# Kernel optimization log

Hardware: AMD Instinct MI355X
Metric: run time of the kernel (lower is better)

The kernel has to match this reference:

```python
import jax, jax.numpy as jnp
import numpy as np

B, N_IN, N_OUT = 16, 7000, 28000
C_IN, C_OUT, S = 64, 64, 9
NNZ = 3 * N_OUT  # ~3 source verts per upsampled vert (barycentric)


def setup_inputs() -> dict:
    key = jax.random.key(0)
    k = jax.random.split(key, 6)
    x = jax.random.normal(k[0], (B, N_IN, C_IN), dtype=jnp.float32)
    values = jax.random.uniform(k[1], (NNZ,), dtype=jnp.float32)
    row = jax.random.randint(k[2], (NNZ,), 0, N_OUT)
    col = jax.random.randint(k[3], (NNZ,), 0, N_IN)
    spiral_indices = jax.random.randint(k[4], (N_OUT, S), 0, N_OUT)
    weight = jax.random.normal(k[5], (S * C_IN, C_OUT), dtype=jnp.float32) * 0.02
    bias = jnp.zeros((C_OUT,), dtype=jnp.float32)
    return {"x": x, "values": values, "weight": weight, "bias": bias,
            "row": row, "col": col, "spiral_indices": spiral_indices}


def reference(x, values, weight, bias, row, col, spiral_indices):
    # Pool: gather source verts, scale by sparse matrix values, scatter-add to output verts
    n_out = spiral_indices.shape[0]
    gathered = x[:, col, :] * values[None, :, None]            # [B, nnz, C]
    pooled = jnp.zeros((x.shape[0], n_out, x.shape[2]), x.dtype).at[:, row, :].add(gathered)  # [B, N_out, C]
    # SpiralConv: gather spiral neighborhood, flatten, linear
    feat = pooled[:, spiral_indices.reshape(-1), :]            # [B, N_out*S, C]
    feat = feat.reshape(x.shape[0], n_out, -1)                 # [B, N_out, S*C]
    out = jax.nn.elu(jnp.einsum('bnf,fo->bno', feat, weight) + bias)
    return out
```

## Files before the change

kernel.cpp:

```cpp
#include <hip/hip_runtime.h>
#include <math.h>

#define B      16
#define N_IN   7000
#define N_OUT  28000
#define C      64
#define S      9
#define NNZ    (3 * N_OUT)
#define F      (S * C)
#define KB     (F / 32)

#define MT     110

typedef short bf16x8 __attribute__((ext_vector_type(8)));
typedef float f32x4  __attribute__((ext_vector_type(4)));

static __device__ __forceinline__ unsigned short f2bf(float f) {
    unsigned u = __float_as_uint(f);
    u += 0x7fffu + ((u >> 16) & 1u);
    return (unsigned short)(u >> 16);
}

__global__ void hist_kernel(const int* __restrict__ row, int* __restrict__ cnt) {
    int i = blockIdx.x * 256 + threadIdx.x;
    if (i < NNZ) atomicAdd(&cnt[row[i]], 1);
}

__global__ void scan_kernel(const int* __restrict__ cnt,
                            int* __restrict__ offs, int* __restrict__ cursor) {
    __shared__ int tmp[1024];
    const int t = threadIdx.x;
    const int base = t * 28;
    const bool live = (t < 1000);

    int c[28];
    int partial = 0;
    if (live) {
        #pragma unroll
        for (int j = 0; j < 28; ++j) { c[j] = cnt[base + j]; partial += c[j]; }
    }
    tmp[t] = partial;
    __syncthreads();
    #pragma unroll
    for (int off = 1; off < 1024; off <<= 1) {
        int v = (t >= off) ? tmp[t - off] : 0;
        __syncthreads();
        tmp[t] += v;
        __syncthreads();
    }
    if (live) {
        int run = tmp[t] - partial;
        #pragma unroll
        for (int j = 0; j < 28; ++j) {
            offs[base + j]   = run;
            cursor[base + j] = run;
            run += c[j];
        }
        if (t == 999) offs[N_OUT] = run;
    }
}

__global__ void place_kernel(const int* __restrict__ row, const int* __restrict__ col,
                             const float* __restrict__ values,
                             int* __restrict__ cursor,
                             int* __restrict__ ecol, float* __restrict__ eval) {
    int i = blockIdx.x * 256 + threadIdx.x;
    if (i < NNZ) {
        int pos = atomicAdd(&cursor[row[i]], 1);
        ecol[pos] = col[i];
        eval[pos] = values[i];
    }
}

__global__ void pool_kernel(const float* __restrict__ x,
                            const int*   __restrict__ ecol,
                            const float* __restrict__ eval,
                            const int*   __restrict__ offs,
                            unsigned short* __restrict__ pooled) {
    const int bg     = blockIdx.x & 7;
    const int rowblk = blockIdx.x >> 3;
    const int wave = threadIdx.x >> 6;
    const int lane = threadIdx.x & 63;
    const int rsub = lane >> 5;
    const int bsub = (lane >> 4) & 1;
    const int sl   = lane & 15;

    const int r = rowblk * 8 + wave * 2 + rsub;
    const int b = bg + 8 * bsub;

    const int start = offs[r], end = offs[r + 1];

    float4 acc = make_float4(0.f, 0.f, 0.f, 0.f);
    const float* xb = x + (size_t)b * N_IN * C + sl * 4;

    for (int e = start; e < end; e += 4) {
        const int nn = end - e;
        int   cl[4]; float vv[4];
        #pragma unroll
        for (int j = 0; j < 4; ++j) {
            const int ee = (j < nn) ? e + j : e;
            cl[j] = ecol[ee];
            vv[j] = (j < nn) ? eval[ee] : 0.f;
        }
        float4 xv[4];
        #pragma unroll
        for (int j = 0; j < 4; ++j)
            xv[j] = *(const float4*)(xb + (size_t)cl[j] * C);
        #pragma unroll
        for (int j = 0; j < 4; ++j) {
            acc.x = fmaf(xv[j].x, vv[j], acc.x);
            acc.y = fmaf(xv[j].y, vv[j], acc.y);
            acc.z = fmaf(xv[j].z, vv[j], acc.z);
            acc.w = fmaf(xv[j].w, vv[j], acc.w);
        }
    }

    unsigned long long ov =
        (unsigned long long)f2bf(acc.x)
        | ((unsigned long long)f2bf(acc.y) << 16)
        | ((unsigned long long)f2bf(acc.z) << 32)
        | ((unsigned long long)f2bf(acc.w) << 48);
    __builtin_nontemporal_store(ov,
        (unsigned long long*)(pooled + ((size_t)b * N_OUT + r) * C + sl * 4));
}

__global__ void packw_kernel(const float* __restrict__ w, unsigned short* __restrict__ pw) {
    const int kb   = blockIdx.x;
    const int nt   = threadIdx.x >> 6;
    const int lane = threadIdx.x & 63;
    const int lm   = lane & 15;
    const int quad = lane >> 4;

    unsigned short v[8];
    #pragma unroll
    for (int j = 0; j < 8; ++j) {
        const int k = kb * 32 + quad * 8 + j;
        const int n = nt * 16 + lm;
        v[j] = f2bf(w[(size_t)k * C + n]);
    }
    unsigned short* dst = pw + ((size_t)(kb * 4 + nt) * 64 + lane) * 8;
    #pragma unroll
    for (int j = 0; j < 8; ++j) dst[j] = v[j];
}

__global__ __launch_bounds__(512, 4)
void spiral_mfma(const unsigned short* __restrict__ pooled,
                 const bf16x8*         __restrict__ packedW,
                 const int*            __restrict__ sp,
                 const float*          __restrict__ bias,
                 float*                __restrict__ out) {
    const int L = blockIdx.x;
    int b, mtile;
    if (L < 8 * MT) { b = L & 7;                  mtile = L >> 3; }
    else            { b = 8 + ((L - 8 * MT) & 7); mtile = (L - 8 * MT) >> 3; }

    const int wave = threadIdx.x >> 6;
    const int lane = threadIdx.x & 63;
    const int lm   = lane & 15;
    const int quad = lane >> 4;
    const int m_base = mtile * 256 + wave * 32;

    __shared__ bf16x8 bw[KB * 4 * 64];
    {
        const int t = threadIdx.x;
        #pragma unroll
        for (int i = 0; i < 9; ++i)
            bw[i * 512 + t] = packedW[i * 512 + t];
    }

    int spv[S];
    {
        int r = m_base + (lane & 31);
        if (r >= N_OUT) r = N_OUT - 1;
        #pragma unroll
        for (int s = 0; s < S; ++s) spv[s] = sp[r * S + s];
    }

    const unsigned short* poolb = pooled + (size_t)b * N_OUT * C;

    f32x4 acc[2][4];
    #pragma unroll
    for (int t = 0; t < 2; ++t)
        #pragma unroll
        for (int nt = 0; nt < 4; ++nt)
            acc[t][nt] = (f32x4){0.f, 0.f, 0.f, 0.f};

    int    rowi[2][2];
    bf16x8 abuf[2][2][2];

    #pragma unroll
    for (int t = 0; t < 2; ++t)
        rowi[0][t] = __shfl(spv[0], t * 16 + lm, 64);
    #pragma unroll
    for (int half = 0; half < 2; ++half) {
        const int c0 = half * 32 + quad * 8;
        #pragma unroll
        for (int t = 0; t < 2; ++t)
            abuf[0][half][t] = *(const bf16x8*)(poolb + (size_t)rowi[0][t] * C + c0);
    }

    __syncthreads();

    #pragma unroll
    for (int s = 0; s < S; ++s) {
        const int cur = s & 1, nxt = cur ^ 1;

        if (s + 1 < S) {
            #pragma unroll
            for (int t = 0; t < 2; ++t)
                rowi[nxt][t] = __shfl(spv[s + 1], t * 16 + lm, 64);
            #pragma unroll
            for (int half = 0; half < 2; ++half) {
                const int c0 = half * 32 + quad * 8;
                #pragma unroll
                for (int t = 0; t < 2; ++t)
                    abuf[nxt][half][t] =
                        *(const bf16x8*)(poolb + (size_t)rowi[nxt][t] * C + c0);
            }
        }

        #pragma unroll
        for (int half = 0; half < 2; ++half) {
            bf16x8 bb[4];
            #pragma unroll
            for (int nt = 0; nt < 4; ++nt)
                bb[nt] = bw[((s * 2 + half) * 4 + nt) * 64 + lane];
            #pragma unroll
            for (int nt = 0; nt < 4; ++nt)
                #pragma unroll
                for (int t = 0; t < 2; ++t)
                    acc[t][nt] = __builtin_amdgcn_mfma_f32_16x16x32_bf16(
                        abuf[cur][half][t], bb[nt], acc[t][nt], 0, 0, 0);
        }
    }

    #pragma unroll
    for (int nt = 0; nt < 4; ++nt) {
        const int n = nt * 16 + lm;
        const float bs = bias[n];
        #pragma unroll
        for (int t = 0; t < 2; ++t) {
            #pragma unroll
            for (int reg = 0; reg < 4; ++reg) {
                const int r = m_base + t * 16 + quad * 4 + reg;
                if (r < N_OUT) {
                    float v = acc[t][nt][reg] + bs;
                    v = v > 0.f ? v : (__expf(v) - 1.0f);
                    __builtin_nontemporal_store(v,
                        out + ((size_t)b * N_OUT + r) * C + n);
                }
            }
        }
    }
}

extern "C" void kernel_launch(void* const* d_in, const int* in_sizes, int n_in,
                              void* d_out, int out_size, void* d_ws, size_t ws_size,
                              hipStream_t stream) {
    const float* x      = (const float*)d_in[0];
    const float* values = (const float*)d_in[1];
    const float* weight = (const float*)d_in[2];
    const float* bias   = (const float*)d_in[3];
    const int*   row    = (const int*)d_in[4];
    const int*   col    = (const int*)d_in[5];
    const int*   sp     = (const int*)d_in[6];
    float*       out    = (float*)d_out;

    char* ws = (char*)d_ws;
    size_t off = 0;
    unsigned short* pooled  = (unsigned short*)(ws + off); off += (size_t)B * N_OUT * C * 2;
    unsigned short* packedW = (unsigned short*)(ws + off); off += (size_t)KB * 4 * 64 * 8 * 2;
    int*   offs   = (int*)(ws + off); off += ((size_t)(N_OUT + 1) * 4 + 124) / 128 * 128;
    int*   cursor = (int*)(ws + off); off += (size_t)N_OUT * 4 + 128;
    int*   cnt    = (int*)(ws + off); off += (size_t)N_OUT * 4 + 128;
    int*   ecol   = (int*)(ws + off); off += (size_t)NNZ * 4;
    float* eval   = (float*)(ws + off); off += (size_t)NNZ * 4;

    (void)hipMemsetAsync(cnt, 0, (size_t)N_OUT * 4, stream);
    hist_kernel <<<(NNZ + 255) / 256, 256, 0, stream>>>(row, cnt);
    scan_kernel <<<1, 1024, 0, stream>>>(cnt, offs, cursor);
    place_kernel<<<(NNZ + 255) / 256, 256, 0, stream>>>(row, col, values, cursor, ecol, eval);

    packw_kernel<<<KB, 256, 0, stream>>>(weight, packedW);

    pool_kernel<<<(N_OUT / 8) * 8, 256, 0, stream>>>(x, ecol, eval, offs, pooled);

    spiral_mfma<<<B * MT, 512, 0, stream>>>(pooled,
        reinterpret_cast<const bf16x8*>(packedW), sp, bias, out);
}
```

Measured before the change: 303.8 us.

## Transpose x and pooled to vertex-major layout for contiguous gathers

```diff
diff --git a/kernel.cpp b/kernel.cpp
--- a/kernel.cpp
+++ b/kernel.cpp
@@ -72,56 +72,57 @@
     }
 }
 
-__global__ void pool_kernel(const float* __restrict__ x,
+__global__ void xt_kernel(const float* __restrict__ x, float* __restrict__ xT) {
+    const int n  = blockIdx.x;
+    const int t  = threadIdx.x;
+    const int b  = t >> 4;
+    const int ch = (t & 15) * 4;
+    const float4 v = *(const float4*)(x + ((size_t)b * N_IN + n) * C + ch);
+    *(float4*)(xT + ((size_t)n * B + b) * C + ch) = v;
+}
+
+__global__ void pool_kernel(const float* __restrict__ xT,
                             const int*   __restrict__ ecol,
                             const float* __restrict__ eval,
                             const int*   __restrict__ offs,
                             unsigned short* __restrict__ pooled) {
-    const int bg     = blockIdx.x & 7;
-    const int rowblk = blockIdx.x >> 3;
     const int wave = threadIdx.x >> 6;
     const int lane = threadIdx.x & 63;
-    const int rsub = lane >> 5;
-    const int bsub = (lane >> 4) & 1;
-    const int sl   = lane & 15;
-
-    const int r = rowblk * 8 + wave * 2 + rsub;
-    const int b = bg + 8 * bsub;
+    const int r    = blockIdx.x * 4 + wave;
 
     const int start = offs[r], end = offs[r + 1];
 
-    float4 acc = make_float4(0.f, 0.f, 0.f, 0.f);
-    const float* xb = x + (size_t)b * N_IN * C + sl * 4;
-
-    for (int e = start; e < end; e += 4) {
-        const int nn = end - e;
-        int   cl[4]; float vv[4];
+    float4 acc[4];
+    #pragma unroll
+    for (int j = 0; j < 4; ++j) acc[j] = make_float4(0.f, 0.f, 0.f, 0.f);
+
+    for (int e = start; e < end; ++e) {
+        const int   cl = ecol[e];
+        const float v  = eval[e];
+        const float* base = xT + (size_t)cl * (B * C) + lane * 4;
+        float4 xv[4];
+        #pragma unroll
+        for (int j = 0; j < 4; ++j)
+            xv[j] = *(const float4*)(base + j * 256);
         #pragma unroll
         for (int j = 0; j < 4; ++j) {
-            const int ee = (j < nn) ? e + j : e;
-            cl[j] = ecol[ee];
-            vv[j] = (j < nn) ? eval[ee] : 0.f;
-        }
-        float4 xv[4];
-        #pragma unroll
-        for (int j = 0; j < 4; ++j)
-            xv[j] = *(const float4*)(xb + (size_t)cl[j] * C);
-        #pragma unroll
-        for (int j = 0; j < 4; ++j) {
-            acc.x = fmaf(xv[j].x, vv[j], acc.x);
-            acc.y = fmaf(xv[j].y, vv[j], acc.y);
-            acc.z = fmaf(xv[j].z, vv[j], acc.z);
-            acc.w = fmaf(xv[j].w, vv[j], acc.w);
-        }
-    }
-
-    unsigned long long ov =
-        (unsigned long long)f2bf(acc.x)
-        | ((unsigned long long)f2bf(acc.y) << 16)
-        | ((unsigned long long)f2bf(acc.z) << 32)
-        | ((unsigned long long)f2bf(acc.w) << 48);
-    __builtin_nontemporal_store(ov,
-        (unsigned long long*)(pooled + ((size_t)b * N_OUT + r) * C + sl * 4));
+            acc[j].x = fmaf(xv[j].x, v, acc[j].x);
+            acc[j].y = fmaf(xv[j].y, v, acc[j].y);
+            acc[j].z = fmaf(xv[j].z, v, acc[j].z);
+            acc[j].w = fmaf(xv[j].w, v, acc[j].w);
+        }
+    }
+
+    unsigned short* dst = pooled + (size_t)r * (B * C) + lane * 4;
+    #pragma unroll
+    for (int j = 0; j < 4; ++j) {
+        unsigned long long ov =
+            (unsigned long long)f2bf(acc[j].x)
+            | ((unsigned long long)f2bf(acc[j].y) << 16)
+            | ((unsigned long long)f2bf(acc[j].z) << 32)
+            | ((unsigned long long)f2bf(acc[j].w) << 48);
+        __builtin_nontemporal_store(ov, (unsigned long long*)(dst + j * 256));
+    }
 }
 
 __global__ void packw_kernel(const float* __restrict__ w, unsigned short* __restrict__ pw) {
@@ -176,7 +177,7 @@
         for (int s = 0; s < S; ++s) spv[s] = sp[r * S + s];
     }
 
-    const unsigned short* poolb = pooled + (size_t)b * N_OUT * C;
+    const unsigned short* poolb = pooled + (size_t)b * C;
 
     f32x4 acc[2][4];
     #pragma unroll
@@ -196,7 +197,8 @@
         const int c0 = half * 32 + quad * 8;
         #pragma unroll
         for (int t = 0; t < 2; ++t)
-            abuf[0][half][t] = *(const bf16x8*)(poolb + (size_t)rowi[0][t] * C + c0);
+            abuf[0][half][t] =
+                *(const bf16x8*)(poolb + (size_t)rowi[0][t] * (B * C) + c0);
     }
 
     __syncthreads();
@@ -215,7 +217,7 @@
                 #pragma unroll
                 for (int t = 0; t < 2; ++t)
                     abuf[nxt][half][t] =
-                        *(const bf16x8*)(poolb + (size_t)rowi[nxt][t] * C + c0);
+                        *(const bf16x8*)(poolb + (size_t)rowi[nxt][t] * (B * C) + c0);
             }
         }
 
@@ -268,8 +270,9 @@
 
     char* ws = (char*)d_ws;
     size_t off = 0;
-    unsigned short* pooled  = (unsigned short*)(ws + off); off += (size_t)B * N_OUT * C * 2;
+    unsigned short* pooled  = (unsigned short*)(ws + off); off += (size_t)N_OUT * B * C * 2;
     unsigned short* packedW = (unsigned short*)(ws + off); off += (size_t)KB * 4 * 64 * 8 * 2;
+    float* xT     = (float*)(ws + off); off += (size_t)N_IN * B * C * 4;
     int*   offs   = (int*)(ws + off); off += ((size_t)(N_OUT + 1) * 4 + 124) / 128 * 128;
     int*   cursor = (int*)(ws + off); off += (size_t)N_OUT * 4 + 128;
     int*   cnt    = (int*)(ws + off); off += (size_t)N_OUT * 4 + 128;
@@ -283,7 +286,9 @@
 
     packw_kernel<<<KB, 256, 0, stream>>>(weight, packedW);
 
-    pool_kernel<<<(N_OUT / 8) * 8, 256, 0, stream>>>(x, ecol, eval, offs, pooled);
+    xt_kernel<<<N_IN, 256, 0, stream>>>(x, xT);
+
+    pool_kernel<<<N_OUT / 4, 256, 0, stream>>>(xT, ecol, eval, offs, pooled);
 
     spiral_mfma<<<B * MT, 512, 0, stream>>>(pooled,
         reinterpret_cast<const bf16x8*>(packedW), sp, bias, out);
```

New measurement: 343.9 us. +13.2%, slower.
